# Kernel tuning notes

Hardware: AMD Instinct MI355X
Metric: run time of the kernel (lower is better)

The kernel has to match this reference:

```python
import jax, jax.numpy as jnp
import numpy as np
from jax.scipy.special import logsumexp

B, L, M, D = 8192, 1024, 128, 2  # batch, hilbert.size, bond dim, local_size
MACHINE_POW = 2


def setup_inputs() -> dict:
    key = jax.random.key(0)
    k1, k2 = jax.random.split(key)
    # configurations in the zero-magnetization sector: each row is a permutation
    # of L//2 zeros and L//2 ones (constrained HomogeneousHilbert)
    base = jnp.tile(jnp.arange(D, dtype=jnp.int32), L // D)  # (L,)
    inputs = jax.vmap(lambda k: jax.random.permutation(k, base))(jax.random.split(k1, B))
    # variational parameters epsilon: (local_size, M, size); centered at 1 so the
    # length-L multiplicative cache chain stays in fp32 range
    epsilon = 1.0 + 0.02 * jax.random.normal(k2, (D, M, L), dtype=jnp.float32)
    return {"inputs": inputs, "epsilon": epsilon}


def _conditionals(inputs, epsilon):
    # inputs: (B, L) int in [0, D); epsilon: (D, M, L)
    Bn, Ln = inputs.shape
    Dn, Mn, _ = epsilon.shape
    half = Ln // 2

    def scan_fun(carry, index):
        cache, n_spins = carry                       # (B, D, M), (B, D)
        prev = inputs[:, (index - 1) % Ln]           # (B,) previous-site state
        params_i = epsilon[:, :, index]              # (D, M)
        # irregular gather: cache[b, prev[b], :]
        gathered = jnp.take_along_axis(cache, prev[:, None, None], axis=1)[:, 0, :]  # (B, M)
        prods = params_i[None, :, :] * gathered[:, None, :]  # (B, D, M)
        log_psi = jnp.sum(prods, axis=-1)            # (B, D) sum over bond dim
        n_spins = jnp.where(index > 0,
                            n_spins + jax.nn.one_hot(prev, Dn, dtype=jnp.int32),
                            n_spins)
        # zero-magnetization renormalization: -inf once a local state is exhausted
        renorm = jnp.log(jnp.heaviside((half - n_spins).astype(log_psi.dtype), 0.0))
        return (prods, n_spins), log_psi + renorm

    cache0 = jnp.ones((Bn, Dn, Mn), epsilon.dtype)
    n0 = jnp.zeros((Bn, Dn), jnp.int32)
    _, log_psi = jax.lax.scan(scan_fun, (cache0, n0), jnp.arange(Ln))
    return jnp.transpose(log_psi, (1, 0, 2))  # (B, L, D)


def reference(inputs, epsilon):
    lp = _conditionals(inputs, epsilon)  # (B, L, D)
    # normalize conditionals over local states (machine_pow = 2)
    lp = lp - (1.0 / MACHINE_POW) * logsumexp(MACHINE_POW * lp, axis=-1, keepdims=True)
    # pick the log-conditional of the actual configuration at each site
    sel = jnp.take_along_axis(lp, inputs[:, :, None], axis=2)[:, :, 0]  # (B, L)
    # n_symm = 1 (default apply_symmetries): symmetrized logsumexp is identity
    return jnp.sum(sel, axis=1)  # (B,) log_psi
```

## Files before the change

### kernel.cpp

```cpp
#include <hip/hip_runtime.h>
#include <hip/hip_fp16.h>

typedef unsigned long long u64;
typedef unsigned int uint32;
typedef short short8 __attribute__((ext_vector_type(8)));
typedef float f32x4 __attribute__((ext_vector_type(4)));
typedef _Float16 h2 __attribute__((ext_vector_type(2)));

#define B_N 8192
#define L_N 1024
#define M_N 128
#define C_N 16
#define CH_N 64
#define HALF_N 512

#define OFF_W16  0
#define OFF_R16  0x40000
#define OFF_BITS 0x80000
#define OFF_LR   0x180000
#define OFF_RQ   0x1C0000
#define OFF_T    0x21C0000

#define PACK_BLK (B_N * L_N / 256)
#define EPS_BLK  32
#define ZERO_BLK 32

__device__ __forceinline__ unsigned short f32_bf16(float f) {
    union { float f; unsigned u; } x; x.f = f;
    unsigned u = x.u + 0x7FFFu + ((x.u >> 16) & 1u);
    return (unsigned short)(u >> 16);
}

__device__ __forceinline__ float fdot2(h2 a, h2 b, float c) {
#if __has_builtin(__builtin_amdgcn_fdot2)
    return __builtin_amdgcn_fdot2(a, b, c, false);
#else
    return (float)a[0] * (float)b[0] + (float)a[1] * (float)b[1] + c;
#endif
}

union HU { uint32 u; __half2 hh; h2 v2; };

__global__ __launch_bounds__(256) void k_prep(const int* __restrict__ inp,
        const float* __restrict__ eps, u64* __restrict__ bits,
        _Float16* __restrict__ w16, _Float16* __restrict__ r16,
        unsigned short* __restrict__ lrT, float* __restrict__ out) {
    int bid = blockIdx.x;
    if (bid < PACK_BLK) {
        int g = bid * 256 + threadIdx.x;
        int v = inp[g];
        u64 m = __ballot(v != 0);
        if ((threadIdx.x & 63) == 0) bits[g >> 6] = m;
        return;
    }
    bid -= PACK_BLK;
    if (bid < EPS_BLK) {
        int wid = threadIdx.x >> 6, lane = threadIdx.x & 63;
        int m = bid * 4 + wid;
        const float* e0 = eps + (size_t)m * L_N + lane * 16;
        const float* e1 = eps + (size_t)(M_N + m) * L_N + lane * 16;
        float a[16], b[16];
        #pragma unroll
        for (int j = 0; j < 16; j += 4) {
            *(float4*)&a[j] = *(const float4*)&e0[j];
            *(float4*)&b[j] = *(const float4*)&e1[j];
        }
        float local = 1.f;
        #pragma unroll
        for (int j = 0; j < 16; ++j) local *= a[j];
        float sc = local;
        #pragma unroll
        for (int d = 1; d < 64; d <<= 1) {
            float up = __shfl_up(sc, d);
            if (lane >= d) sc *= up;
        }
        float prev = __shfl_up(sc, 1);
        float E = (lane == 0) ? 1.f : prev;
        int i0 = lane * 16;
        #pragma unroll
        for (int j = 0; j < 16; ++j) {
            float rat = b[j] / a[j];
            w16[(size_t)(i0 + j) * M_N + m] = (_Float16)(E * (a[j] - b[j]));
            r16[(size_t)(i0 + j) * M_N + m] = (_Float16)rat;
            lrT[(size_t)m * L_N + i0 + j] = f32_bf16(__log2f(rat));
            E *= a[j];
        }
        return;
    }
    bid -= EPS_BLK;
    if (bid < ZERO_BLK) {
        out[bid * 256 + threadIdx.x] = 0.f;
    }
}

__global__ __launch_bounds__(256) void k_slog2(const u64* __restrict__ bits,
        const unsigned short* __restrict__ lrT, _Float16* __restrict__ Rq,
        int* __restrict__ T) {
    if (blockIdx.x >= 1024) {
        int b = (blockIdx.x - 1024) * 256 + threadIdx.x;
        const u64* brow = bits + (size_t)b * 16;
        int n1 = 0, n0 = 0, Tv = 1024;
        for (int wd = 0; wd < 16; ++wd) {
            u64 x = brow[wd];
            int pc = __popcll(x);
            if (n1 + pc < HALF_N && n0 + (64 - pc) < HALF_N) {
                n1 += pc; n0 += 64 - pc;
                continue;
            }
            int found = 0;
            for (int k = 0; k < 64; ++k) {
                if (n1 >= HALF_N || n0 >= HALF_N) { Tv = wd * 64 + k; found = 1; break; }
                int sb = (int)((x >> k) & 1);
                n1 += sb; n0 += 1 - sb;
            }
            if (!found) Tv = (wd + 1) * 64;
            break;
        }
        T[b] = Tv;
        return;
    }
    int btile = blockIdx.x >> 1;
    int half = blockIdx.x & 1;
    int wid = threadIdx.x >> 6, lane = threadIdx.x & 63;
    int col = lane & 15, quad = lane >> 4;
    int m = (half * 4 + wid) * 16 + col;
    int b_row = btile * 16 + col;
    const u64* brow = bits + (size_t)b_row * 16;
    const unsigned short* lrow = lrT + (size_t)m * L_N;

    f32x4 cum = (f32x4){0.f, 0.f, 0.f, 0.f};

    for (int c = 0; c < C_N; ++c) {
        #pragma unroll
        for (int reg = 0; reg < 4; ++reg) {
            int b = btile * 16 + quad * 4 + reg;
            Rq[((size_t)c * B_N + b) * M_N + m] = (_Float16)exp2f(cum[reg]);
        }
        u64 wv = brow[c];
        short8 a0, a1;
        #pragma unroll
        for (int j = 0; j < 8; ++j) {
            a0[j] = (short)((((wv >> (quad * 8 + j)) & 1) != 0) ? 0x3F80 : 0);
            a1[j] = (short)((((wv >> (32 + quad * 8 + j)) & 1) != 0) ? 0x3F80 : 0);
        }
        const unsigned short* bp = lrow + c * 64 + quad * 8;
        union { uint4 u; short8 s; } bf0, bf1;
        bf0.u = *(const uint4*)bp;
        bf1.u = *(const uint4*)(bp + 32);
        cum = __builtin_amdgcn_mfma_f32_16x16x32_bf16(a0, bf0.s, cum, 0, 0, 0);
        cum = __builtin_amdgcn_mfma_f32_16x16x32_bf16(a1, bf1.s, cum, 0, 0, 0);
    }
}

__global__ __launch_bounds__(256, 2) void k_main(const u64* __restrict__ bits,
        const _Float16* __restrict__ w16, const _Float16* __restrict__ r16,
        const _Float16* __restrict__ Rq, const int* __restrict__ T,
        float* __restrict__ out) {
    __shared__ _Float16 wbuf[CH_N * M_N];
    __shared__ _Float16 rbuf[CH_N * M_N];
    int c = blockIdx.x & (C_N - 1);
    int bblk = blockIdx.x >> 4;
    int lane = threadIdx.x & 63, wid = threadIdx.x >> 6;
    int s = lane & 7, g = lane >> 3;
    int b0 = bblk * 128 + wid * 32 + g * 4;
    int b_own = b0 + (s & 3);

    {
        const uint4* sw = (const uint4*)(w16 + (size_t)c * CH_N * M_N);
        const uint4* sr = (const uint4*)(r16 + (size_t)c * CH_N * M_N);
        uint4* dw = (uint4*)wbuf; uint4* dr = (uint4*)rbuf;
        #pragma unroll
        for (int t = 0; t < 4; ++t) {
            dw[threadIdx.x + t * 256] = sw[threadIdx.x + t * 256];
            dr[threadIdx.x + t * 256] = sr[threadIdx.x + t * 256];
        }
    }

    HU R2[4][8];
    #pragma unroll
    for (int nb = 0; nb < 4; ++nb) {
        union { uint4 q[2]; uint32 w[8]; } P;
        const uint4* src = (const uint4*)(Rq + ((size_t)c * B_N + (b0 + nb)) * M_N + s * 16);
        P.q[0] = src[0]; P.q[1] = src[1];
        #pragma unroll
        for (int j = 0; j < 8; ++j) R2[nb][j].u = P.w[j];
    }
    int Tb = T[b_own];
    u64 wb[4];
    #pragma unroll
    for (int nb = 0; nb < 4; ++nb) wb[nb] = bits[(size_t)(b0 + nb) * 16 + c];

    __syncthreads();

    const uint32 ONE2 = 0x3C003C00u;
    const float LOG2E2 = 2.885390082f;
    const float NHL2 = -0.3465735903f;
    float sum = 0.f;
    #pragma unroll
    for (int h = 0; h < 2; ++h) {
        uint32 wh[4];
        #pragma unroll
        for (int nb = 0; nb < 4; ++nb) wh[nb] = (uint32)(wb[nb] >> (h * 32));
        uint32 owa = (s & 1) ? wh[1] : wh[0];
        uint32 owb = (s & 1) ? wh[3] : wh[2];
        uint32 ow = (s & 2) ? owb : owa;

        int rel = Tb - (c * CH_N + h * 32);
        uint32 vmask = (rel <= 0) ? 0u : ((rel >= 32) ? 0xFFFFFFFFu : ((1u << rel) - 1u));

        for (int tt = 0; tt < 32; ++tt) {
            int base = (h * 32 + tt) * M_N + s * 16;
            union { uint4 q[2]; uint32 w[8]; h2 v2[8]; } W;
            union { uint4 q[2]; uint32 w[8]; } Rr;
            W.q[0] = *(const uint4*)&wbuf[base];
            W.q[1] = *((const uint4*)&wbuf[base] + 1);
            Rr.q[0] = *(const uint4*)&rbuf[base];
            Rr.q[1] = *((const uint4*)&rbuf[base] + 1);

            float d[4];
            #pragma unroll
            for (int nb = 0; nb < 4; ++nb) {
                float acc = 0.f;
                #pragma unroll
                for (int j = 0; j < 8; ++j) acc = fdot2(R2[nb][j].v2, W.v2[j], acc);
                d[nb] = acc;
            }
            float xa = (s & 1) ? d[1] : d[0];
            float ya = (s & 1) ? d[0] : d[1];
            xa += __shfl_xor(ya, 1);
            float xb = (s & 1) ? d[3] : d[2];
            float yb = (s & 1) ? d[2] : d[3];
            xb += __shfl_xor(yb, 1);
            float u2 = (s & 2) ? xb : xa;
            float v2 = (s & 2) ? xa : xb;
            u2 += __shfl_xor(v2, 2);
            u2 += __shfl_xor(u2, 4);
            float Dv = u2;

            int sbit = (ow >> tt) & 1;
            float y = sbit ? Dv : -Dv;
            float contr = NHL2 * __log2f(1.f + exp2f(LOG2E2 * y));
            sum += ((vmask >> tt) & 1) ? contr : 0.f;

            #pragma unroll
            for (int nb = 0; nb < 4; ++nb) {
                bool bit = (wh[nb] >> tt) & 1;
                #pragma unroll
                for (int j = 0; j < 8; ++j) {
                    HU sel; sel.u = bit ? Rr.w[j] : ONE2;
                    R2[nb][j].hh = __hmul2(R2[nb][j].hh, sel.hh);
                }
            }
        }
    }
    if (s < 4) atomicAdd(&out[b_own], sum);
}

extern "C" void kernel_launch(void* const* d_in, const int* in_sizes, int n_in,
                              void* d_out, int out_size, void* d_ws, size_t ws_size,
                              hipStream_t stream) {
    const int*   inputs  = (const int*)d_in[0];
    const float* epsilon = (const float*)d_in[1];
    float* out = (float*)d_out;

    char* ws = (char*)d_ws;
    _Float16* w16 = (_Float16*)(ws + OFF_W16);
    _Float16* r16 = (_Float16*)(ws + OFF_R16);
    u64*   bits   = (u64*)  (ws + OFF_BITS);
    unsigned short* lrT = (unsigned short*)(ws + OFF_LR);
    _Float16* Rq  = (_Float16*)(ws + OFF_RQ);
    int*   T      = (int*)  (ws + OFF_T);

    k_prep<<<PACK_BLK + EPS_BLK + ZERO_BLK, 256, 0, stream>>>(
        inputs, epsilon, bits, w16, r16, lrT, out);
    k_slog2<<<1024 + 32, 256, 0, stream>>>(bits, lrT, Rq, T);
    k_main<<<(B_N / 128) * C_N, 256, 0, stream>>>(bits, w16, r16, Rq, T, out);
}
```

Baseline: 182.8 us.

## Halve per-thread batch rows in main kernel, use DPP reductions and branchless masks

The main kernel now handles 2 batch rows per 8-lane group instead of 4, doubling the grid and halving the R2 register state. The cross-lane reductions move from shuffles to DPP row operations. Sign flips and validity selects become bitmask operations, and the ratio update becomes R += (r-1)*R with a bitmask, using r-1 stored in fp16. The pack kernel is also changed to loop over 16 elements per thread with fewer blocks. The intent is less register pressure, fewer instructions per step and cheaper reductions, at the cost of reloading the LDS chunk for twice as many blocks.

```diff
diff --git a/kernel.cpp b/kernel.cpp
--- a/kernel.cpp
+++ b/kernel.cpp
@@ -21,7 +21,8 @@
 #define OFF_RQ   0x1C0000
 #define OFF_T    0x21C0000
 
-#define PACK_BLK (B_N * L_N / 256)
+#define PACK_BLK 2048
+#define PACK_IT  16
 #define EPS_BLK  32
 #define ZERO_BLK 32
 
@@ -37,6 +38,17 @@
 #else
     return (float)a[0] * (float)b[0] + (float)a[1] * (float)b[1] + c;
 #endif
+}
+
+__device__ __forceinline__ uint32 fas_u(float f) { union { float f; uint32 u; } x; x.f = f; return x.u; }
+__device__ __forceinline__ float uas_f(uint32 u) { union { uint32 u; float f; } x; x.u = u; return x.f; }
+
+template<int CTRL>
+__device__ __forceinline__ float dpp_add(float x, float y) {
+    union { float f; int i; } a, r;
+    a.f = y;
+    r.i = __builtin_amdgcn_update_dpp(0, a.i, CTRL, 0xF, 0xF, true);
+    return x + r.f;
 }
 
 union HU { uint32 u; __half2 hh; h2 v2; };
@@ -48,9 +60,14 @@
     int bid = blockIdx.x;
     if (bid < PACK_BLK) {
         int g = bid * 256 + threadIdx.x;
-        int v = inp[g];
-        u64 m = __ballot(v != 0);
-        if ((threadIdx.x & 63) == 0) bits[g >> 6] = m;
+        const int stride = PACK_BLK * 256;
+        #pragma unroll 4
+        for (int it = 0; it < PACK_IT; ++it) {
+            int v = inp[g];
+            u64 m = __ballot(v != 0);
+            if ((threadIdx.x & 63) == 0) bits[g >> 6] = m;
+            g += stride;
+        }
         return;
     }
     bid -= PACK_BLK;
@@ -81,7 +98,7 @@
         for (int j = 0; j < 16; ++j) {
             float rat = b[j] / a[j];
             w16[(size_t)(i0 + j) * M_N + m] = (_Float16)(E * (a[j] - b[j]));
-            r16[(size_t)(i0 + j) * M_N + m] = (_Float16)rat;
+            r16[(size_t)(i0 + j) * M_N + m] = (_Float16)(rat - 1.f);
             lrT[(size_t)m * L_N + i0 + j] = f32_bf16(__log2f(rat));
             E *= a[j];
         }
@@ -162,8 +179,8 @@
     int bblk = blockIdx.x >> 4;
     int lane = threadIdx.x & 63, wid = threadIdx.x >> 6;
     int s = lane & 7, g = lane >> 3;
-    int b0 = bblk * 128 + wid * 32 + g * 4;
-    int b_own = b0 + (s & 3);
+    int b0 = bblk * 64 + wid * 16 + g * 2;
+    int b_own = b0 + (s & 1);
 
     {
         const uint4* sw = (const uint4*)(w16 + (size_t)c * CH_N * M_N);
@@ -176,9 +193,9 @@
         }
     }
 
-    HU R2[4][8];
+    HU R2[2][8];
     #pragma unroll
-    for (int nb = 0; nb < 4; ++nb) {
+    for (int nb = 0; nb < 2; ++nb) {
         union { uint4 q[2]; uint32 w[8]; } P;
         const uint4* src = (const uint4*)(Rq + ((size_t)c * B_N + (b0 + nb)) * M_N + s * 16);
         P.q[0] = src[0]; P.q[1] = src[1];
@@ -186,40 +203,35 @@
         for (int j = 0; j < 8; ++j) R2[nb][j].u = P.w[j];
     }
     int Tb = T[b_own];
-    u64 wb[4];
-    #pragma unroll
-    for (int nb = 0; nb < 4; ++nb) wb[nb] = bits[(size_t)(b0 + nb) * 16 + c];
+    u64 wb[2];
+    wb[0] = bits[(size_t)b0 * 16 + c];
+    wb[1] = bits[(size_t)(b0 + 1) * 16 + c];
 
     __syncthreads();
 
-    const uint32 ONE2 = 0x3C003C00u;
     const float LOG2E2 = 2.885390082f;
     const float NHL2 = -0.3465735903f;
     float sum = 0.f;
     #pragma unroll
     for (int h = 0; h < 2; ++h) {
-        uint32 wh[4];
-        #pragma unroll
-        for (int nb = 0; nb < 4; ++nb) wh[nb] = (uint32)(wb[nb] >> (h * 32));
-        uint32 owa = (s & 1) ? wh[1] : wh[0];
-        uint32 owb = (s & 1) ? wh[3] : wh[2];
-        uint32 ow = (s & 2) ? owb : owa;
-
+        uint32 wh[2];
+        wh[0] = (uint32)(wb[0] >> (h * 32));
+        wh[1] = (uint32)(wb[1] >> (h * 32));
+        uint32 ows = ~((s & 1) ? wh[1] : wh[0]);
         int rel = Tb - (c * CH_N + h * 32);
         uint32 vmask = (rel <= 0) ? 0u : ((rel >= 32) ? 0xFFFFFFFFu : ((1u << rel) - 1u));
 
         for (int tt = 0; tt < 32; ++tt) {
             int base = (h * 32 + tt) * M_N + s * 16;
-            union { uint4 q[2]; uint32 w[8]; h2 v2[8]; } W;
-            union { uint4 q[2]; uint32 w[8]; } Rr;
+            union { uint4 q[2]; uint32 w[8]; h2 v2[8]; } W, Rm;
             W.q[0] = *(const uint4*)&wbuf[base];
             W.q[1] = *((const uint4*)&wbuf[base] + 1);
-            Rr.q[0] = *(const uint4*)&rbuf[base];
-            Rr.q[1] = *((const uint4*)&rbuf[base] + 1);
-
-            float d[4];
+            Rm.q[0] = *(const uint4*)&rbuf[base];
+            Rm.q[1] = *((const uint4*)&rbuf[base] + 1);
+
+            float d[2];
             #pragma unroll
-            for (int nb = 0; nb < 4; ++nb) {
+            for (int nb = 0; nb < 2; ++nb) {
                 float acc = 0.f;
                 #pragma unroll
                 for (int j = 0; j < 8; ++j) acc = fdot2(R2[nb][j].v2, W.v2[j], acc);
@@ -227,33 +239,28 @@
             }
             float xa = (s & 1) ? d[1] : d[0];
             float ya = (s & 1) ? d[0] : d[1];
-            xa += __shfl_xor(ya, 1);
-            float xb = (s & 1) ? d[3] : d[2];
-            float yb = (s & 1) ? d[2] : d[3];
-            xb += __shfl_xor(yb, 1);
-            float u2 = (s & 2) ? xb : xa;
-            float v2 = (s & 2) ? xa : xb;
-            u2 += __shfl_xor(v2, 2);
-            u2 += __shfl_xor(u2, 4);
-            float Dv = u2;
-
-            int sbit = (ow >> tt) & 1;
-            float y = sbit ? Dv : -Dv;
+            xa = dpp_add<0xB1>(xa, ya);
+            xa = dpp_add<0x4E>(xa, xa);
+            xa = dpp_add<0x104>(xa, xa);
+
+            uint32 sgn = (ows << (31 - tt)) & 0x80000000u;
+            float y = uas_f(fas_u(xa) ^ sgn);
             float contr = NHL2 * __log2f(1.f + exp2f(LOG2E2 * y));
-            sum += ((vmask >> tt) & 1) ? contr : 0.f;
+            int vm = (int)(vmask << (31 - tt)) >> 31;
+            sum += uas_f(fas_u(contr) & (uint32)vm);
 
             #pragma unroll
-            for (int nb = 0; nb < 4; ++nb) {
-                bool bit = (wh[nb] >> tt) & 1;
+            for (int nb = 0; nb < 2; ++nb) {
+                uint32 msk = (uint32)((int)(wh[nb] << (31 - tt)) >> 31);
                 #pragma unroll
                 for (int j = 0; j < 8; ++j) {
-                    HU sel; sel.u = bit ? Rr.w[j] : ONE2;
-                    R2[nb][j].hh = __hmul2(R2[nb][j].hh, sel.hh);
+                    HU sel; sel.u = Rm.w[j] & msk;
+                    R2[nb][j].v2 += sel.v2 * R2[nb][j].v2;
                 }
             }
         }
     }
-    if (s < 4) atomicAdd(&out[b_own], sum);
+    if (s < 2) atomicAdd(&out[b_own], sum);
 }
 
 extern "C" void kernel_launch(void* const* d_in, const int* in_sizes, int n_in,
@@ -274,5 +281,5 @@
     k_prep<<<PACK_BLK + EPS_BLK + ZERO_BLK, 256, 0, stream>>>(
         inputs, epsilon, bits, w16, r16, lrT, out);
     k_slog2<<<1024 + 32, 256, 0, stream>>>(bits, lrT, Rq, T);
-    k_main<<<(B_N / 128) * C_N, 256, 0, stream>>>(bits, w16, r16, Rq, T, out);
-}
+    k_main<<<(B_N / 64) * C_N, 256, 0, stream>>>(bits, w16, r16, Rq, T, out);
+}
```

Measured after the change: 179.8 us. About the same (-1.6%).
